# Kernel tuning notes

Measured on AMD Instinct MI355X. Metric: run time of the kernel, lower is better.

## Reference

```python
import jax, jax.numpy as jnp
import numpy as np
import math
from itertools import permutations

B, C_IN, C_OUT, K, N, D, F_DIM = 2, 4, 8, 4, 224, 2, 128


def _make_perms(k):
    # [k!, k, k] permutation matrices, same ordering as itertools.permutations
    nP = math.factorial(k)
    perms = np.zeros((nP, k, k), dtype=np.float32)
    for c, p in enumerate(permutations(range(k))):
        perms[c, np.arange(k), np.array(p)] = 1.0
    return jnp.asarray(perms)


def setup_inputs() -> dict:
    key = jax.random.key(0)
    ks = jax.random.split(key, 6)
    graph = jax.random.normal(ks[0], (B, C_IN, N, N), jnp.float32)
    types = jax.random.normal(ks[1], (B, C_IN, N), jnp.float32)
    features = jax.random.normal(ks[2], (B, N, F_DIM), jnp.float32)
    # xavier-uniform-ish scales for the learned kernels
    k_struct = jax.random.normal(ks[3], (C_OUT, C_IN, K, K), jnp.float32) * 0.3
    k_row = jax.random.normal(ks[4], (C_OUT, C_IN, K), jnp.float32) * 0.5
    k_col = jax.random.normal(ks[5], (C_OUT, C_IN, K), jnp.float32) * 0.5
    return {"graph": graph, "types": types, "features": features,
            "k_struct": k_struct, "k_row": k_row, "k_col": k_col}


def _forward(graph, types, features, k_struct, k_row, k_col):
    Bn, C, Nn, _ = graph.shape
    k = k_struct.shape[-1]
    new_k = (k - 1) * D + 1
    nH = Nn - new_k + 1            # square graph -> nW == nH
    n_sub = nH * nH
    idx = jnp.arange(nH)[:, None] + jnp.arange(k) * D  # [nH, k] dilated window indices

    # --- _prepare: dilated subgraph extraction (vectorized gather) ---
    g = graph[:, :, idx, :]            # [B,C,nH,k,N]
    g = g[..., idx]                    # [B,C,nH,k,nH,k]
    sub = jnp.transpose(g, (0, 2, 4, 1, 3, 5)).reshape(Bn, n_sub, C, k, k)
    rt = jnp.transpose(types[:, :, idx], (0, 2, 1, 3))  # [B,nH,C,k]
    row_t = jnp.broadcast_to(rt[:, :, None], (Bn, nH, nH, C, k)).reshape(Bn, n_sub, C, k)
    col_t = jnp.broadcast_to(rt[:, None, :], (Bn, nH, nH, C, k)).reshape(Bn, n_sub, C, k)
    rf = features[:, idx, :].sum(axis=-2)              # [B,nH,F]
    feats = rf[:, :, None, :] + rf[:, None, :, :]      # row_features + col_features
    h_mean = feats.reshape(Bn, n_sub, -1).mean(axis=1)  # [B,F]

    # --- permuted kernels ---
    perms = _make_perms(k)                                  # [P,k,k]
    Kp = jnp.einsum('pau,oiuv,pbv->oipab', perms, k_struct, perms)  # P K P^T
    Rp = jnp.einsum('pau,oiu->oipa', perms, k_row)
    Cp = jnp.einsum('pau,oiu->oipa', perms, k_col)

    subf = sub.reshape(-1, C, k, k)   # [n,i,a,b], n = B*n_sub
    rtf = row_t.reshape(-1, C, k)
    ctf = col_t.reshape(-1, C, k)

    # ||X - Y||_F^2 = ||X||^2 + ||Y||^2 - 2<X,Y>, avoids the huge broadcasted diff
    def sq_dist(x2_ni, y2_opi, cross_nopi):
        return y2_opi[None] + x2_ni[:, None, None, :] - 2.0 * cross_nopi

    G2 = jnp.sum(subf * subf, axis=(-2, -1))                       # [n,i]
    K2 = jnp.transpose(jnp.sum(Kp * Kp, axis=(-2, -1)), (0, 2, 1))  # [o,p,i]
    struct = sq_dist(G2, K2, jnp.einsum('niab,oipab->nopi', subf, Kp))
    R2 = jnp.transpose(jnp.sum(Rp * Rp, axis=-1), (0, 2, 1))
    rsim = sq_dist(jnp.sum(rtf * rtf, axis=-1), R2, jnp.einsum('nia,oipa->nopi', rtf, Rp))
    C2 = jnp.transpose(jnp.sum(Cp * Cp, axis=-1), (0, 2, 1))
    csim = sq_dist(jnp.sum(ctf * ctf, axis=-1), C2, jnp.einsum('nia,oipa->nopi', ctf, Cp))

    total = struct + rsim + csim            # [n, o, P, i]
    # maxpool over P of (-total), negated back == min over permutations of total
    pooled = jnp.min(total, axis=2)         # [n, o, i]
    sims = jnp.transpose(pooled.reshape(Bn, n_sub, -1), (0, 2, 1))  # [B, o*i, n_sub]
    out_sim = (1.0 - jax.nn.softmax(sims, axis=-1)) / sims.shape[-1]
    return h_mean, out_sim


def reference(graph, types, features, k_struct, k_row, k_col):
    return _forward(graph, types, features, k_struct, k_row, k_col)
```

## Files before the change

### kernel.cpp

```cpp
#include <hip/hip_runtime.h>
#include <hip/hip_bf16.h>

#define B_    2
#define CIN   4
#define COUT  8
#define KK    4
#define DD    2
#define NN    224
#define FDIM  128
#define NH    218
#define NSUB  (NH*NH)
#define NPERM 24
#define NROWS (B_*COUT*CIN)
#define CHUNK 1984
#define MB    ((NSUB + CHUNK - 1) / CHUNK)

__device__ static constexpr int PERM[NPERM][4] = {
  {0,1,2,3},{0,1,3,2},{0,2,1,3},{0,2,3,1},{0,3,1,2},{0,3,2,1},
  {1,0,2,3},{1,0,3,2},{1,2,0,3},{1,2,3,0},{1,3,0,2},{1,3,2,0},
  {2,0,1,3},{2,0,3,1},{2,1,0,3},{2,1,3,0},{2,3,0,1},{2,3,1,0},
  {3,0,1,2},{3,0,2,1},{3,1,0,2},{3,1,2,0},{3,2,0,1},{3,2,1,0}
};

__global__ __launch_bounds__(64) void hmean_kernel(const float* __restrict__ features,
                                                   float* __restrict__ out) {
  int bf = blockIdx.x;
  int b = bf / FDIM, f = bf - b * FDIM;
  int lane = threadIdx.x;
  const float* fb = features + (size_t)b * NN * FDIM + f;
  float acc = 0.f;
  for (int r = lane; r < NN; r += 64) {
    int w = 0;
#pragma unroll
    for (int a = 0; a < KK; ++a) {
      int i0 = r - a * DD;
      if (0 <= i0 && i0 < NH) w++;
    }
    acc += (float)w * fb[(size_t)r * FDIM];
  }
#pragma unroll
  for (int off = 32; off > 0; off >>= 1) acc += __shfl_down(acc, off, 64);
  if (lane == 0) out[bf] = acc * (2.0f / (float)NH);
}

__global__ __launch_bounds__(256) void sims_kernel(
    const float* __restrict__ graph, const float* __restrict__ types,
    const float* __restrict__ ksA, const float* __restrict__ krA,
    const float* __restrict__ kcA, float* __restrict__ simsOut)
{
  __shared__ float ls[COUT * CIN * 16];
  __shared__ float lr[COUT * CIN * 4];
  __shared__ float lc[COUT * CIN * 4];
  int t = threadIdx.x;
  for (int i = t; i < COUT * CIN * 16; i += 256) ls[i] = ksA[i];
  for (int i = t; i < COUT * CIN * 4; i += 256) { lr[i] = krA[i]; lc[i] = kcA[i]; }
  __syncthreads();

  int gid = blockIdx.x * 256 + t;
  if (gid >= B_ * CIN * NSUB) return;
  int bci = gid / NSUB;
  int s   = gid - bci * NSUB;
  int b   = bci / CIN;
  int ci  = bci - b * CIN;
  int ii  = s / NH;
  int jj  = s - ii * NH;

  const float* gi = graph + ((size_t)b * CIN + ci) * NN * NN;
  const float* ti = types + ((size_t)b * CIN + ci) * NN;

  float subv[16], rtv[4], ctv[4];
  float G2 = 0.f, T2r = 0.f, T2c = 0.f;
#pragma unroll
  for (int a = 0; a < KK; ++a) {
    const float* row = gi + (size_t)(ii + a * DD) * NN + jj;
#pragma unroll
    for (int bb = 0; bb < KK; ++bb) {
      float v = row[bb * DD];
      subv[a * 4 + bb] = v;
      G2 += v * v;
    }
    float rv = ti[ii + a * DD];
    float cv = ti[jj + a * DD];
    rtv[a] = rv; ctv[a] = cv;
    T2r += rv * rv; T2c += cv * cv;
  }
  float base0 = G2 + T2r + T2c;

#pragma unroll 1
  for (int o = 0; o < COUT; ++o) {
    float kS[16], kR[4], kC[4];
    const float4* pS4 = (const float4*)(ls + (o * CIN + ci) * 16);
    const float* pR = lr + (o * CIN + ci) * 4;
    const float* pC = lc + (o * CIN + ci) * 4;
    float K2 = 0.f;
#pragma unroll
    for (int u = 0; u < 4; ++u) {
      float4 v4 = pS4[u];
      kS[u*4+0] = v4.x; kS[u*4+1] = v4.y; kS[u*4+2] = v4.z; kS[u*4+3] = v4.w;
      K2 += v4.x*v4.x + v4.y*v4.y + v4.z*v4.z + v4.w*v4.w;
    }
#pragma unroll
    for (int u = 0; u < 4; ++u) {
      kR[u] = pR[u]; kC[u] = pC[u];
      K2 += kR[u] * kR[u] + kC[u] * kC[u];
    }
    float base = base0 + K2;
    float best = 3.4e38f;
#pragma unroll
    for (int p = 0; p < NPERM; ++p) {
      float cr = 0.f;
#pragma unroll
      for (int a = 0; a < 4; ++a) {
#pragma unroll
        for (int bb = 0; bb < 4; ++bb)
          cr += subv[a * 4 + bb] * kS[PERM[p][a] * 4 + PERM[p][bb]];
        cr += rtv[a] * kR[PERM[p][a]] + ctv[a] * kC[PERM[p][a]];
      }
      float tot = base - 2.f * cr;
      best = fminf(best, tot);
    }
    simsOut[(((size_t)b * COUT + o) * CIN + ci) * NSUB + s] = best;
  }
}

__global__ __launch_bounds__(256) void softmax_partial(const float* __restrict__ sims,
                                                       float* __restrict__ partial) {
  int blk = blockIdx.x;
  int row = blk / MB;
  int ch  = blk - row * MB;
  int base = ch * CHUNK;
  int n = NSUB - base; if (n > CHUNK) n = CHUNK;
  const float* rp = sims + (size_t)row * NSUB + base;
  int t = threadIdx.x;

  float v[8]; int cnt = 0;
  for (int i = t; i < n; i += 256) v[cnt++] = rp[i];

  __shared__ float red[256];
  float m = -3.4e38f;
  for (int u = 0; u < cnt; ++u) m = fmaxf(m, v[u]);
  red[t] = m; __syncthreads();
  for (int off = 128; off > 0; off >>= 1) {
    if (t < off) red[t] = fmaxf(red[t], red[t + off]);
    __syncthreads();
  }
  m = red[0]; __syncthreads();
  float l = 0.f;
  for (int u = 0; u < cnt; ++u) l += __expf(v[u] - m);
  red[t] = l; __syncthreads();
  for (int off = 128; off > 0; off >>= 1) {
    if (t < off) red[t] += red[t + off];
    __syncthreads();
  }
  if (t == 0) { partial[2 * blk] = m; partial[2 * blk + 1] = red[0]; }
}

__global__ __launch_bounds__(64) void softmax_combine(const float* __restrict__ partial,
                                                      float* __restrict__ stats) {
  int row = blockIdx.x;
  int t = threadIdx.x;
  float m = -3.4e38f, l = 0.f;
  if (t < MB) { m = partial[2 * (row * MB + t)]; l = partial[2 * (row * MB + t) + 1]; }
#pragma unroll
  for (int off = 32; off > 0; off >>= 1) m = fmaxf(m, __shfl_down(m, off, 64));
  m = __shfl(m, 0, 64);
  float contrib = (t < MB) ? l * __expf(partial[2 * (row * MB + t)] - m) : 0.f;
#pragma unroll
  for (int off = 32; off > 0; off >>= 1) contrib += __shfl_down(contrib, off, 64);
  if (t == 0) { stats[2 * row] = m; stats[2 * row + 1] = 1.0f / contrib; }
}

__global__ __launch_bounds__(256) void softmax_final(float* __restrict__ sims,
                                                     const float* __restrict__ stats) {
  int blk = blockIdx.x;
  int row = blk / MB;
  int ch  = blk - row * MB;
  int base = ch * CHUNK;
  int n = NSUB - base; if (n > CHUNK) n = CHUNK;
  float* rp = sims + (size_t)row * NSUB + base;
  float M = stats[2 * row], invS = stats[2 * row + 1];
  const float scale = 1.0f / (float)NSUB;
  for (int i = threadIdx.x; i < n; i += 256) {
    float e = __expf(rp[i] - M) * invS;
    rp[i] = (1.0f - e) * scale;
  }
}

extern "C" void kernel_launch(void* const* d_in, const int* in_sizes, int n_in,
                              void* d_out, int out_size, void* d_ws, size_t ws_size,
                              hipStream_t stream) {
  const float* graph    = (const float*)d_in[0];
  const float* types    = (const float*)d_in[1];
  const float* features = (const float*)d_in[2];
  const float* ks       = (const float*)d_in[3];
  const float* kr       = (const float*)d_in[4];
  const float* kc       = (const float*)d_in[5];
  float* out  = (float*)d_out;
  float* sims = out + B_ * FDIM;

  float* partial = (float*)d_ws;
  float* stats   = partial + NROWS * MB * 2;

  hmean_kernel<<<B_ * FDIM, 64, 0, stream>>>(features, out);
  int total = B_ * CIN * NSUB;
  sims_kernel<<<(total + 255) / 256, 256, 0, stream>>>(graph, types, ks, kr, kc, sims);
  softmax_partial<<<NROWS * MB, 256, 0, stream>>>(sims, partial);
  softmax_combine<<<NROWS, 64, 0, stream>>>(partial, stats);
  softmax_final<<<NROWS * MB, 256, 0, stream>>>(sims, stats);
}
```

Baseline: 120.8 us.

## Factor diagonal/type terms per permutation, split output channels across threads, vectorize softmax

The sims kernel precomputes a 4x4 table of diagonal-structure plus row/col type products, so each permutation needs only four table lookups plus the twelve off-diagonal products. It also moves the per-kernel norm K2 into shared memory, computed once per block. Output channels are split into four groups handled by separate threads, giving four times more threads with less serial work each. The softmax passes now use float4 loads and stores with new chunk sizes. More threads recompute the same subgraph loads, and the float4 path assumes NSUB is divisible by 4, which holds for 218*218.

```diff
diff --git a/kernel.cpp b/kernel.cpp
--- a/kernel.cpp
+++ b/kernel.cpp
@@ -12,8 +12,10 @@
 #define NSUB  (NH*NH)
 #define NPERM 24
 #define NROWS (B_*COUT*CIN)
-#define CHUNK 1984
-#define MB    ((NSUB + CHUNK - 1) / CHUNK)
+#define NSUB4 (NSUB/4)
+#define CH4   512
+#define MB    ((NSUB4 + CH4 - 1) / CH4)
+#define OG    4
 
 __device__ static constexpr int PERM[NPERM][4] = {
   {0,1,2,3},{0,1,3,2},{0,2,1,3},{0,2,3,1},{0,3,1,2},{0,3,2,1},
@@ -51,15 +53,27 @@
   __shared__ float ls[COUT * CIN * 16];
   __shared__ float lr[COUT * CIN * 4];
   __shared__ float lc[COUT * CIN * 4];
+  __shared__ float lK2[COUT * CIN];
   int t = threadIdx.x;
   for (int i = t; i < COUT * CIN * 16; i += 256) ls[i] = ksA[i];
   for (int i = t; i < COUT * CIN * 4; i += 256) { lr[i] = krA[i]; lc[i] = kcA[i]; }
   __syncthreads();
-
-  int gid = blockIdx.x * 256 + t;
-  if (gid >= B_ * CIN * NSUB) return;
-  int bci = gid / NSUB;
-  int s   = gid - bci * NSUB;
+  if (t < COUT * CIN) {
+    float k2 = 0.f;
+#pragma unroll
+    for (int u = 0; u < 16; ++u) k2 += ls[t * 16 + u] * ls[t * 16 + u];
+#pragma unroll
+    for (int u = 0; u < 4; ++u) k2 += lr[t * 4 + u] * lr[t * 4 + u] + lc[t * 4 + u] * lc[t * 4 + u];
+    lK2[t] = k2;
+  }
+  __syncthreads();
+
+  long long gid = (long long)blockIdx.x * 256 + t;
+  if (gid >= (long long)OG * B_ * CIN * NSUB) return;
+  int ogbci = (int)(gid / NSUB);
+  int s     = (int)(gid - (long long)ogbci * NSUB);
+  int og  = ogbci / (B_ * CIN);
+  int bci = ogbci - og * (B_ * CIN);
   int b   = bci / CIN;
   int ci  = bci - b * CIN;
   int ii  = s / NH;
@@ -86,39 +100,41 @@
   }
   float base0 = G2 + T2r + T2c;
 
-#pragma unroll 1
-  for (int o = 0; o < COUT; ++o) {
+#pragma unroll
+  for (int oo = 0; oo < COUT / OG; ++oo) {
+    int o = og + oo * OG;
+    int oc = o * CIN + ci;
+    const float* pS = ls + oc * 16;
+    const float* pR = lr + oc * 4;
+    const float* pC = lc + oc * 4;
     float kS[16], kR[4], kC[4];
-    const float4* pS4 = (const float4*)(ls + (o * CIN + ci) * 16);
-    const float* pR = lr + (o * CIN + ci) * 4;
-    const float* pC = lc + (o * CIN + ci) * 4;
-    float K2 = 0.f;
-#pragma unroll
-    for (int u = 0; u < 4; ++u) {
-      float4 v4 = pS4[u];
-      kS[u*4+0] = v4.x; kS[u*4+1] = v4.y; kS[u*4+2] = v4.z; kS[u*4+3] = v4.w;
-      K2 += v4.x*v4.x + v4.y*v4.y + v4.z*v4.z + v4.w*v4.w;
+#pragma unroll
+    for (int u = 0; u < 16; ++u) kS[u] = pS[u];
+#pragma unroll
+    for (int u = 0; u < 4; ++u) { kR[u] = pR[u]; kC[u] = pC[u]; }
+
+    float C1[16];
+#pragma unroll
+    for (int a = 0; a < 4; ++a)
+#pragma unroll
+      for (int ap = 0; ap < 4; ++ap)
+        C1[a * 4 + ap] = subv[a * 4 + a] * kS[ap * 4 + ap]
+                       + rtv[a] * kR[ap] + ctv[a] * kC[ap];
+
+    float maxcr = -3.4e38f;
+#pragma unroll
+    for (int p = 0; p < NPERM; ++p) {
+      float cr = C1[0 * 4 + PERM[p][0]] + C1[1 * 4 + PERM[p][1]]
+               + C1[2 * 4 + PERM[p][2]] + C1[3 * 4 + PERM[p][3]];
+#pragma unroll
+      for (int a = 0; a < 4; ++a)
+#pragma unroll
+        for (int bb = 0; bb < 4; ++bb)
+          if (a != bb)
+            cr += subv[a * 4 + bb] * kS[PERM[p][a] * 4 + PERM[p][bb]];
+      maxcr = fmaxf(maxcr, cr);
     }
-#pragma unroll
-    for (int u = 0; u < 4; ++u) {
-      kR[u] = pR[u]; kC[u] = pC[u];
-      K2 += kR[u] * kR[u] + kC[u] * kC[u];
-    }
-    float base = base0 + K2;
-    float best = 3.4e38f;
-#pragma unroll
-    for (int p = 0; p < NPERM; ++p) {
-      float cr = 0.f;
-#pragma unroll
-      for (int a = 0; a < 4; ++a) {
-#pragma unroll
-        for (int bb = 0; bb < 4; ++bb)
-          cr += subv[a * 4 + bb] * kS[PERM[p][a] * 4 + PERM[p][bb]];
-        cr += rtv[a] * kR[PERM[p][a]] + ctv[a] * kC[PERM[p][a]];
-      }
-      float tot = base - 2.f * cr;
-      best = fminf(best, tot);
-    }
+    float best = base0 + lK2[oc] - 2.0f * maxcr;
     simsOut[(((size_t)b * COUT + o) * CIN + ci) * NSUB + s] = best;
   }
 }
@@ -128,17 +144,18 @@
   int blk = blockIdx.x;
   int row = blk / MB;
   int ch  = blk - row * MB;
-  int base = ch * CHUNK;
-  int n = NSUB - base; if (n > CHUNK) n = CHUNK;
-  const float* rp = sims + (size_t)row * NSUB + base;
+  int base4 = ch * CH4;
+  int n4 = NSUB4 - base4; if (n4 > CH4) n4 = CH4;
+  const float4* rp = (const float4*)(sims + (size_t)row * NSUB) + base4;
   int t = threadIdx.x;
 
-  float v[8]; int cnt = 0;
-  for (int i = t; i < n; i += 256) v[cnt++] = rp[i];
+  float4 v[2]; int cnt = 0;
+  for (int i = t; i < n4; i += 256) v[cnt++] = rp[i];
 
   __shared__ float red[256];
   float m = -3.4e38f;
-  for (int u = 0; u < cnt; ++u) m = fmaxf(m, v[u]);
+  for (int u = 0; u < cnt; ++u)
+    m = fmaxf(fmaxf(fmaxf(m, v[u].x), fmaxf(v[u].y, v[u].z)), v[u].w);
   red[t] = m; __syncthreads();
   for (int off = 128; off > 0; off >>= 1) {
     if (t < off) red[t] = fmaxf(red[t], red[t + off]);
@@ -146,7 +163,8 @@
   }
   m = red[0]; __syncthreads();
   float l = 0.f;
-  for (int u = 0; u < cnt; ++u) l += __expf(v[u] - m);
+  for (int u = 0; u < cnt; ++u)
+    l += __expf(v[u].x - m) + __expf(v[u].y - m) + __expf(v[u].z - m) + __expf(v[u].w - m);
   red[t] = l; __syncthreads();
   for (int off = 128; off > 0; off >>= 1) {
     if (t < off) red[t] += red[t + off];
@@ -175,14 +193,18 @@
   int blk = blockIdx.x;
   int row = blk / MB;
   int ch  = blk - row * MB;
-  int base = ch * CHUNK;
-  int n = NSUB - base; if (n > CHUNK) n = CHUNK;
-  float* rp = sims + (size_t)row * NSUB + base;
+  int base4 = ch * CH4;
+  int n4 = NSUB4 - base4; if (n4 > CH4) n4 = CH4;
+  float4* rp = (float4*)(sims + (size_t)row * NSUB) + base4;
   float M = stats[2 * row], invS = stats[2 * row + 1];
   const float scale = 1.0f / (float)NSUB;
-  for (int i = threadIdx.x; i < n; i += 256) {
-    float e = __expf(rp[i] - M) * invS;
-    rp[i] = (1.0f - e) * scale;
+  for (int i = threadIdx.x; i < n4; i += 256) {
+    float4 v = rp[i];
+    v.x = (1.0f - __expf(v.x - M) * invS) * scale;
+    v.y = (1.0f - __expf(v.y - M) * invS) * scale;
+    v.z = (1.0f - __expf(v.z - M) * invS) * scale;
+    v.w = (1.0f - __expf(v.w - M) * invS) * scale;
+    rp[i] = v;
   }
 }
 
@@ -202,8 +224,9 @@
   float* stats   = partial + NROWS * MB * 2;
 
   hmean_kernel<<<B_ * FDIM, 64, 0, stream>>>(features, out);
-  int total = B_ * CIN * NSUB;
-  sims_kernel<<<(total + 255) / 256, 256, 0, stream>>>(graph, types, ks, kr, kc, sims);
+  long long total = (long long)OG * B_ * CIN * NSUB;
+  int nblk = (int)((total + 255) / 256);
+  sims_kernel<<<nblk, 256, 0, stream>>>(graph, types, ks, kr, kc, sims);
   softmax_partial<<<NROWS * MB, 256, 0, stream>>>(sims, partial);
   softmax_combine<<<NROWS, 64, 0, stream>>>(partial, stats);
   softmax_final<<<NROWS * MB, 256, 0, stream>>>(sims, stats);
```

After: 135.5 us. +12.2%, slower.
